# Kernel optimization log

Measured on AMD Instinct MI355X. Metric: run time of the kernel, lower is better.

## Reference

```python
import jax, jax.numpy as jnp
import numpy as np

T, E = 8192, 1024
LAYER_DEPTH, NUM_LAYERS = 12, 24


def _init_params():
    ratio_0_to_1 = LAYER_DEPTH / (NUM_LAYERS - 1)
    ratio_1_to_almost_0 = 1.0 - LAYER_DEPTH / NUM_LAYERS
    zigzag = 0.5 * (jnp.arange(1, E + 1) % 3 - 1)
    time_first = jnp.full(E, jnp.log(0.3), dtype=jnp.float32) + zigzag.astype(jnp.float32)
    h = jnp.arange(0, E, dtype=jnp.float32)
    time_decay = (-5 + 8 * (h / (E - 1)) ** (0.7 + 1.3 * ratio_0_to_1)).astype(jnp.float32)
    xr = jnp.arange(E, dtype=jnp.float32) / E
    time_mix_k = jnp.power(xr, ratio_1_to_almost_0)
    time_mix_v = time_mix_k + 0.3 * ratio_0_to_1
    time_mix_r = jnp.power(xr, 0.5 * ratio_1_to_almost_0)
    return time_first, time_decay, time_mix_k, time_mix_v, time_mix_r


def setup_inputs() -> dict:
    key = jax.random.key(0)
    kx, kk_, kv_, kr_, ko_ = jax.random.split(key, 5)
    scale = 1.0 / np.sqrt(E)
    tf, td, tmk, tmv, tmr = _init_params()
    return {
        "x": jax.random.normal(kx, (T, E), dtype=jnp.float32),
        "sx": jnp.zeros((E,), jnp.float32),
        "aa": jnp.zeros((E,), jnp.float32),
        "bb": jnp.zeros((E,), jnp.float32),
        "pp": jnp.zeros((E,), jnp.float32),
        "time_first": tf,
        "time_decay": td,
        "time_mix_k": tmk,
        "time_mix_v": tmv,
        "time_mix_r": tmr,
        "Wk": jax.random.normal(kk_, (E, E), jnp.float32) * scale,
        "Wv": jax.random.normal(kv_, (E, E), jnp.float32) * scale,
        "Wr": jax.random.normal(kr_, (E, E), jnp.float32) * scale,
        "Wo": jax.random.normal(ko_, (E, E), jnp.float32) * scale,
    }


def reference(x, sx, aa, bb, pp, time_first, time_decay,
              time_mix_k, time_mix_v, time_mix_r, Wk, Wv, Wr, Wo):
    # token-shift: previous token (or carried state sx at t=0)  [T, E]
    sx_seq = jnp.concatenate((sx[None, :], x[:-1, :]), axis=0)
    kx = x * time_mix_k + sx_seq * (1.0 - time_mix_k)
    vx = x * time_mix_v + sx_seq * (1.0 - time_mix_v)
    rx = x * time_mix_r + sx_seq * (1.0 - time_mix_r)

    r = jax.nn.sigmoid(rx @ Wr)  # [T, E]
    k = kx @ Wk                  # [T, E]
    v = vx @ Wv                  # [T, E]
    decay = -jnp.exp(time_decay)  # [E]

    def step(state, kv):
        aa_, bb_, pp_ = state
        kk, vv = kv
        ww = time_first + kk
        p = jnp.maximum(pp_, ww)
        e1 = jnp.exp(pp_ - p)
        e2 = jnp.exp(ww - p)
        out = (e1 * aa_ + e2 * vv) / (e1 * bb_ + e2)
        ww2 = decay + pp_
        p2 = jnp.maximum(ww2, kk)
        e1b = jnp.exp(ww2 - p2)
        e2b = jnp.exp(kk - p2)
        return (e1b * aa_ + e2b * vv, e1b * bb_ + e2b, p2), out

    (aa_f, bb_f, pp_f), wkv = jax.lax.scan(step, (aa, bb, pp), (k, v))
    out = x + (r * wkv) @ Wo
    return out, x[-1, :], aa_f, bb_f, pp_f
```

## Files before the change

### kernel.cpp

```cpp
#include <hip/hip_runtime.h>
#include <cstdint>
#include <cstddef>

typedef __bf16 bf16x8 __attribute__((ext_vector_type(8)));
typedef float  f32x4  __attribute__((ext_vector_type(4)));

#define TT 8192
#define EE 1024
#define NCHUNK 128
#define CLEN 64
#define LDSK 40

__device__ __forceinline__ unsigned short f2bf(float f) {
    union { float f; unsigned int u; } v; v.f = f;
    unsigned int r = v.u + 0x7FFFu + ((v.u >> 16) & 1u);
    return (unsigned short)(r >> 16);
}
__device__ __forceinline__ float b2f(unsigned int h) {
    union { unsigned int u; float f; } v; v.u = h << 16; return v.f;
}
__device__ __forceinline__ void gload_lds16(const void* g, void* l) {
    __builtin_amdgcn_global_load_lds((__attribute__((address_space(1))) void*)g,
                                     (__attribute__((address_space(3))) void*)l, 16, 0, 0);
}

__global__ void wt_kernel(const float* __restrict__ Wk, const float* __restrict__ Wv,
                          const float* __restrict__ Wr, const float* __restrict__ Wo,
                          unsigned short* __restrict__ Tk, unsigned short* __restrict__ Tv,
                          unsigned short* __restrict__ Tr, unsigned short* __restrict__ To) {
    __shared__ float tile[32][33];
    const float* W; unsigned short* D;
    switch (blockIdx.z) {
        case 0:  W = Wk; D = Tk; break;
        case 1:  W = Wv; D = Tv; break;
        case 2:  W = Wr; D = Tr; break;
        default: W = Wo; D = To; break;
    }
    const int bx = blockIdx.x * 32, by = blockIdx.y * 32;
    const int tx = threadIdx.x, ty = threadIdx.y;
#pragma unroll
    for (int r = 0; r < 4; ++r)
        tile[ty + 8 * r][tx] = W[(size_t)(by + ty + 8 * r) * EE + bx + tx];
    __syncthreads();
#pragma unroll
    for (int r = 0; r < 4; ++r)
        D[(size_t)(bx + ty + 8 * r) * EE + by + tx] = f2bf(tile[tx][ty + 8 * r]);
}

__global__ void prep_kernel(const float* __restrict__ Wk, const float* __restrict__ Wv,
                            const float* __restrict__ Wr, const float* __restrict__ Wo,
                            unsigned short* __restrict__ Tk, unsigned short* __restrict__ Tv,
                            unsigned short* __restrict__ Tr, unsigned short* __restrict__ To,
                            const float* __restrict__ x, const float* __restrict__ sx,
                            const float* __restrict__ tmk, const float* __restrict__ tmv,
                            const float* __restrict__ tmr,
                            unsigned short* __restrict__ kxb, unsigned short* __restrict__ vxb,
                            unsigned short* __restrict__ rxb) {
    const int bid = blockIdx.x;
    if (bid < 4096) {
        __shared__ float tile[32][33];
        const int z = bid >> 10;
        const float* W; unsigned short* D;
        switch (z) {
            case 0:  W = Wk; D = Tk; break;
            case 1:  W = Wv; D = Tv; break;
            case 2:  W = Wr; D = Tr; break;
            default: W = Wo; D = To; break;
        }
        const int by = ((bid >> 5) & 31) * 32, bx = (bid & 31) * 32;
        const int tx = threadIdx.x & 31, ty = threadIdx.x >> 5;
#pragma unroll
        for (int r = 0; r < 4; ++r)
            tile[ty + 8 * r][tx] = W[(size_t)(by + ty + 8 * r) * EE + bx + tx];
        __syncthreads();
#pragma unroll
        for (int r = 0; r < 4; ++r)
            D[(size_t)(bx + ty + 8 * r) * EE + by + tx] = f2bf(tile[tx][ty + 8 * r]);
    } else {
        const int gid  = (bid - 4096) * 256 + threadIdx.x;
        const int base = gid * 4;
        const int t = base >> 10;
        const int e = base & (EE - 1);
        float4 xv = *(const float4*)(x + base);
        float4 pv = (t > 0) ? *(const float4*)(x + base - EE) : *(const float4*)(sx + e);
        float4 mk = *(const float4*)(tmk + e);
        float4 mv = *(const float4*)(tmv + e);
        float4 mr = *(const float4*)(tmr + e);
        ushort4 ko, vo, ro;
        ko.x = f2bf(fmaf(mk.x, xv.x - pv.x, pv.x));
        ko.y = f2bf(fmaf(mk.y, xv.y - pv.y, pv.y));
        ko.z = f2bf(fmaf(mk.z, xv.z - pv.z, pv.z));
        ko.w = f2bf(fmaf(mk.w, xv.w - pv.w, pv.w));
        vo.x = f2bf(fmaf(mv.x, xv.x - pv.x, pv.x));
        vo.y = f2bf(fmaf(mv.y, xv.y - pv.y, pv.y));
        vo.z = f2bf(fmaf(mv.z, xv.z - pv.z, pv.z));
        vo.w = f2bf(fmaf(mv.w, xv.w - pv.w, pv.w));
        ro.x = f2bf(fmaf(mr.x, xv.x - pv.x, pv.x));
        ro.y = f2bf(fmaf(mr.y, xv.y - pv.y, pv.y));
        ro.z = f2bf(fmaf(mr.z, xv.z - pv.z, pv.z));
        ro.w = f2bf(fmaf(mr.w, xv.w - pv.w, pv.w));
        *(ushort4*)(kxb + base) = ko;
        *(ushort4*)(vxb + base) = vo;
        *(ushort4*)(rxb + base) = ro;
    }
}

__global__ __launch_bounds__(256, 2) void gemm_kvr3(
        const unsigned short* __restrict__ kxb, const unsigned short* __restrict__ vxb,
        const unsigned short* __restrict__ rxb,
        const unsigned short* __restrict__ Wkt, const unsigned short* __restrict__ Wvt,
        const unsigned short* __restrict__ Wrt,
        unsigned short* __restrict__ kf, unsigned short* __restrict__ vf,
        unsigned short* __restrict__ ry) {
    __shared__ __align__(16) unsigned short As[256 * 32];
    __shared__ __align__(16) unsigned short Bs[128 * 32];
    const int z = blockIdx.z;
    const unsigned short* A  = (z == 0) ? kxb : (z == 1) ? vxb : rxb;
    const unsigned short* Bt = (z == 0) ? Wkt : (z == 1) ? Wvt : Wrt;
    unsigned short* C        = (z == 0) ? kf  : (z == 1) ? vf  : ry;

    const int tid  = threadIdx.x;
    const int wave = tid >> 6, lane = tid & 63;
    const int wm = (wave >> 1) * 128, wn = (wave & 1) * 64;
    const int l15 = lane & 15, lq = lane >> 4;
    const int lrow = lane >> 2, lcol = (lane & 3) * 8;
    const int bm = blockIdx.x * 256, bn = blockIdx.y * 128;

    f32x4 acc[8][4] = {};

    for (int kt = 0; kt < 1024; kt += 32) {
        __syncthreads();
#pragma unroll
        for (int p = 0; p < 4; ++p) {
            const int r0 = p * 64 + wave * 16;
            gload_lds16(A + (size_t)(bm + r0 + lrow) * 1024 + kt + lcol, &As[r0 * 32]);
        }
#pragma unroll
        for (int p = 0; p < 2; ++p) {
            const int r0 = p * 64 + wave * 16;
            gload_lds16(Bt + (size_t)(bn + r0 + lrow) * 1024 + kt + lcol, &Bs[r0 * 32]);
        }
        __syncthreads();
        bf16x8 af[8], bfr[4];
#pragma unroll
        for (int i = 0; i < 8; ++i)
            af[i] = *(const bf16x8*)(&As[(wm + i * 16 + l15) * 32 + lq * 8]);
#pragma unroll
        for (int j = 0; j < 4; ++j)
            bfr[j] = *(const bf16x8*)(&Bs[(wn + j * 16 + l15) * 32 + lq * 8]);
#pragma unroll
        for (int i = 0; i < 8; ++i)
#pragma unroll
            for (int j = 0; j < 4; ++j)
                acc[i][j] = __builtin_amdgcn_mfma_f32_16x16x32_bf16(af[i], bfr[j], acc[i][j], 0, 0, 0);
    }

    const bool sig = (z == 2);
#pragma unroll
    for (int i = 0; i < 8; ++i)
#pragma unroll
        for (int j = 0; j < 4; ++j) {
            const int col = bn + wn + j * 16 + l15;
#pragma unroll
            for (int r = 0; r < 4; ++r) {
                const int row = bm + wm + i * 16 + lq * 4 + r;
                float val = acc[i][j][r];
                if (sig) val = 1.f / (1.f + __expf(-val));
                C[(size_t)row * 1024 + col] = f2bf(val);
            }
        }
}

__global__ __launch_bounds__(256, 2) void gemm_wo_big(const unsigned short* __restrict__ A,
                                                      const unsigned short* __restrict__ Bt,
                                                      const float* __restrict__ Res,
                                                      float* __restrict__ C) {
    __shared__ __align__(16) unsigned short As[256 * 32];
    __shared__ __align__(16) unsigned short Bs[128 * 32];
    const int tid  = threadIdx.x;
    const int wave = tid >> 6, lane = tid & 63;
    const int wm = (wave >> 1) * 128, wn = (wave & 1) * 64;
    const int l15 = lane & 15, lq = lane >> 4;
    const int lrow = lane >> 2, lcol = (lane & 3) * 8;
    const int bm = blockIdx.x * 256, bn = blockIdx.y * 128;

    f32x4 acc[8][4] = {};

    for (int kt = 0; kt < 1024; kt += 32) {
        __syncthreads();
#pragma unroll
        for (int p = 0; p < 4; ++p) {
            const int r0 = p * 64 + wave * 16;
            gload_lds16(A + (size_t)(bm + r0 + lrow) * 1024 + kt + lcol, &As[r0 * 32]);
        }
#pragma unroll
        for (int p = 0; p < 2; ++p) {
            const int r0 = p * 64 + wave * 16;
            gload_lds16(Bt + (size_t)(bn + r0 + lrow) * 1024 + kt + lcol, &Bs[r0 * 32]);
        }
        __syncthreads();
        bf16x8 af[8], bfr[4];
#pragma unroll
        for (int i = 0; i < 8; ++i)
            af[i] = *(const bf16x8*)(&As[(wm + i * 16 + l15) * 32 + lq * 8]);
#pragma unroll
        for (int j = 0; j < 4; ++j)
            bfr[j] = *(const bf16x8*)(&Bs[(wn + j * 16 + l15) * 32 + lq * 8]);
#pragma unroll
        for (int i = 0; i < 8; ++i)
#pragma unroll
            for (int j = 0; j < 4; ++j)
                acc[i][j] = __builtin_amdgcn_mfma_f32_16x16x32_bf16(af[i], bfr[j], acc[i][j], 0, 0, 0);
    }

#pragma unroll
    for (int i = 0; i < 8; ++i)
#pragma unroll
        for (int j = 0; j < 4; ++j) {
            const int col = bn + wn + j * 16 + l15;
#pragma unroll
            for (int r = 0; r < 4; ++r) {
                const int row = bm + wm + i * 16 + lq * 4 + r;
                const size_t idx = (size_t)row * 1024 + col;
                C[idx] = acc[i][j][r] + Res[idx];
            }
        }
}

__global__ __launch_bounds__(256) void gemm_bf(
        const unsigned short* __restrict__ A0, const unsigned short* __restrict__ B0,
        unsigned short* __restrict__ C0, const int sig0,
        const unsigned short* __restrict__ A1, const unsigned short* __restrict__ B1,
        unsigned short* __restrict__ C1, const int sig1) {
    __shared__ __align__(16) unsigned short As[128 * 32];
    __shared__ __align__(16) unsigned short Bs[128 * 32];
    const int z = blockIdx.z;
    const unsigned short* A  = z ? A1 : A0;
    const unsigned short* Bt = z ? B1 : B0;
    unsigned short* C        = z ? C1 : C0;
    const int sig            = z ? sig1 : sig0;

    const int tid  = threadIdx.x;
    const int wave = tid >> 6, lane = tid & 63;
    const int wm = (wave >> 1) * 64, wn = (wave & 1) * 64;
    const int l15 = lane & 15, lq = lane >> 4;
    const int lrow = lane >> 2, lcol = (lane & 3) * 8;
    const int bm = blockIdx.x * 128, bn = blockIdx.y * 128;

    f32x4 acc[4][4] = {};

    for (int kt = 0; kt < 1024; kt += 32) {
        __syncthreads();
#pragma unroll
        for (int p = 0; p < 2; ++p) {
            const int r0 = p * 64 + wave * 16;
            gload_lds16(A  + (size_t)(bm + r0 + lrow) * 1024 + kt + lcol, &As[r0 * 32]);
            gload_lds16(Bt + (size_t)(bn + r0 + lrow) * 1024 + kt + lcol, &Bs[r0 * 32]);
        }
        __syncthreads();
        bf16x8 af[4], bfr[4];
#pragma unroll
        for (int i = 0; i < 4; ++i) {
            af[i]  = *(const bf16x8*)(&As[(wm + i * 16 + l15) * 32 + lq * 8]);
            bfr[i] = *(const bf16x8*)(&Bs[(wn + i * 16 + l15) * 32 + lq * 8]);
        }
#pragma unroll
        for (int i = 0; i < 4; ++i)
#pragma unroll
            for (int j = 0; j < 4; ++j)
                acc[i][j] = __builtin_amdgcn_mfma_f32_16x16x32_bf16(af[i], bfr[j], acc[i][j], 0, 0, 0);
    }

#pragma unroll
    for (int i = 0; i < 4; ++i)
#pragma unroll
        for (int j = 0; j < 4; ++j) {
            const int col = bn + wn + j * 16 + l15;
#pragma unroll
            for (int r = 0; r < 4; ++r) {
                const int row = bm + wm + i * 16 + lq * 4 + r;
                float val = acc[i][j][r];
                if (sig) val = 1.f / (1.f + __expf(-val));
                C[(size_t)row * 1024 + col] = f2bf(val);
            }
        }
}

__global__ __launch_bounds__(256, 4) void gemm_kvr(
        const float* __restrict__ X, const float* __restrict__ SX,
        const float* __restrict__ tmk, const float* __restrict__ tmv,
        const float* __restrict__ tmr,
        const unsigned short* __restrict__ Wkt, const unsigned short* __restrict__ Wvt,
        const unsigned short* __restrict__ Wrt,
        unsigned short* __restrict__ outK, unsigned short* __restrict__ outV,
        unsigned short* __restrict__ outR) {
    __shared__ __align__(16) unsigned short As[128 * LDSK];
    __shared__ __align__(16) unsigned short Bs[128 * LDSK];
    const int z = blockIdx.z;
    const float* TM = (z == 0) ? tmk : (z == 1) ? tmv : tmr;
    const unsigned short* Bt = (z == 0) ? Wkt : (z == 1) ? Wvt : Wrt;
    unsigned short* Cout = (z == 0) ? outK : (z == 1) ? outV : outR;

    const int tid  = threadIdx.x;
    const int wave = tid >> 6, lane = tid & 63;
    const int wm = (wave >> 1) * 64, wn = (wave & 1) * 64;
    const int l15 = lane & 15, lq = lane >> 4;
    const int bm = blockIdx.x * 128, bn = blockIdx.y * 128;

    f32x4 acc[4][4] = {};

    for (int kt = 0; kt < 1024; kt += 32) {
        __syncthreads();
#pragma unroll
        for (int p = 0; p < 2; ++p) {
            const int li  = p * 256 + tid;
            const int row = li >> 2, q = li & 3;
            const int e0  = kt + q * 8;
            {
                const int t = bm + row;
                const float* xr = X + (size_t)t * EE + e0;
                const float* pr = (t > 0) ? (X + (size_t)(t - 1) * EE + e0) : (SX + e0);
                float4 xa = *(const float4*)xr, xb = *(const float4*)(xr + 4);
                float4 pa = *(const float4*)pr, pb = *(const float4*)(pr + 4);
                float4 ma = *(const float4*)(TM + e0), mb = *(const float4*)(TM + e0 + 4);
                ushort4 lo, hi;
                lo.x = f2bf(fmaf(ma.x, xa.x - pa.x, pa.x));
                lo.y = f2bf(fmaf(ma.y, xa.y - pa.y, pa.y));
                lo.z = f2bf(fmaf(ma.z, xa.z - pa.z, pa.z));
                lo.w = f2bf(fmaf(ma.w, xa.w - pa.w, pa.w));
                hi.x = f2bf(fmaf(mb.x, xb.x - pb.x, pb.x));
                hi.y = f2bf(fmaf(mb.y, xb.y - pb.y, pb.y));
                hi.z = f2bf(fmaf(mb.z, xb.z - pb.z, pb.z));
                hi.w = f2bf(fmaf(mb.w, xb.w - pb.w, pb.w));
                *(ushort4*)(&As[row * LDSK + q * 8])     = lo;
                *(ushort4*)(&As[row * LDSK + q * 8 + 4]) = hi;
            }
            *(uint4*)(&Bs[row * LDSK + q * 8]) =
                *(const uint4*)(Bt + (size_t)(bn + row) * 1024 + e0);
        }
        __syncthreads();
        bf16x8 af[4], bfr[4];
#pragma unroll
        for (int i = 0; i < 4; ++i) {
            af[i]  = *(const bf16x8*)(&As[(wm + i * 16 + l15) * LDSK + lq * 8]);
            bfr[i] = *(const bf16x8*)(&Bs[(wn + i * 16 + l15) * LDSK + lq * 8]);
        }
#pragma unroll
        for (int i = 0; i < 4; ++i)
#pragma unroll
            for (int j = 0; j < 4; ++j)
                acc[i][j] = __builtin_amdgcn_mfma_f32_16x16x32_bf16(af[i], bfr[j], acc[i][j], 0, 0, 0);
    }

    const bool sig = (z == 2);
#pragma unroll
    for (int i = 0; i < 4; ++i)
#pragma unroll
        for (int j = 0; j < 4; ++j) {
            const int col = bn + wn + j * 16 + l15;
#pragma unroll
            for (int r = 0; r < 4; ++r) {
                const int row = bm + wm + i * 16 + lq * 4 + r;
                float val = acc[i][j][r];
                if (sig) val = 1.f / (1.f + __expf(-val));
                Cout[(size_t)row * 1024 + col] = f2bf(val);
            }
        }
}

__global__ void wkv_pass_a(const unsigned short* __restrict__ k,
                           const unsigned short* __restrict__ v,
                           const float* __restrict__ td,
                           float* __restrict__ Sa, float* __restrict__ Sb, float* __restrict__ Sp) {
    const int gid = blockIdx.x * 256 + threadIdx.x;
    const int c = gid >> 10, e = gid & (EE - 1);
    const float w = -__expf(td[e]);
    float sa = 0.f, sb = 0.f, sp = -1e30f;
    const size_t base = (size_t)c * CLEN * EE + e;
    for (int i = 0; i < CLEN; ++i) {
        const size_t idx = base + (size_t)i * EE;
        const float kk = b2f(k[idx]), vv = b2f(v[idx]);
        const float q  = fmaf(w, (float)(CLEN - 1 - i), kk);
        const float p2 = fmaxf(sp, q);
        const float e1 = __expf(sp - p2), e2 = __expf(q - p2);
        sa = fmaf(e1, sa, e2 * vv);
        sb = fmaf(e1, sb, e2);
        sp = p2;
    }
    Sa[gid] = sa; Sb[gid] = sb; Sp[gid] = sp;
}

__global__ void wkv_pass_b(const float* __restrict__ aa, const float* __restrict__ bb,
                           const float* __restrict__ pp, const float* __restrict__ td,
                           const float* __restrict__ x,
                           const float* __restrict__ Sa, const float* __restrict__ Sb,
                           const float* __restrict__ Sp,
                           float* __restrict__ ina, float* __restrict__ inb,
                           float* __restrict__ inp, float* __restrict__ outTail) {
    const int e = blockIdx.x * 256 + threadIdx.x;
    const float w  = -__expf(td[e]);
    const float wL = w * (float)CLEN;
    float a = aa[e], b = bb[e], p = pp[e];
    for (int c = 0; c < NCHUNK; ++c) {
        const int idx = c * EE + e;
        ina[idx] = a; inb[idx] = b; inp[idx] = p;
        const float sa = Sa[idx], sb = Sb[idx], sp = Sp[idx];
        const float pw = p + wL;
        const float p2 = fmaxf(pw, sp);
        const float e1 = __expf(pw - p2), e2 = __expf(sp - p2);
        a = fmaf(e1, a, e2 * sa);
        b = fmaf(e1, b, e2 * sb);
        p = p2;
    }
    outTail[e]          = x[(size_t)(TT - 1) * EE + e];
    outTail[EE + e]     = a;
    outTail[2 * EE + e] = b;
    outTail[3 * EE + e] = p;
}

__global__ void wkv_pass_c(const unsigned short* __restrict__ k,
                           const unsigned short* __restrict__ v,
                           const float* __restrict__ tf, const float* __restrict__ td,
                           const float* __restrict__ ina, const float* __restrict__ inb,
                           const float* __restrict__ inp,
                           unsigned short* ry) {
    const int gid = blockIdx.x * 256 + threadIdx.x;
    const int c = gid >> 10, e = gid & (EE - 1);
    const float w = -__expf(td[e]);
    const float u = tf[e];
    float a = ina[gid], b = inb[gid], p = inp[gid];
    const size_t base = (size_t)c * CLEN * EE + e;
    for (int i = 0; i < CLEN; ++i) {
        const size_t idx = base + (size_t)i * EE;
        const float kk = b2f(k[idx]), vv = b2f(v[idx]);
        const float rr = b2f(ry[idx]);
        const float ww = u + kk;
        const float pq = fmaxf(p, ww);
        const float e1 = __expf(p - pq), e2 = __expf(ww - pq);
        const float wkv = fmaf(e1, a, e2 * vv) / fmaf(e1, b, e2);
        ry[idx] = f2bf(rr * wkv);
        const float ww2 = w + p;
        const float p2  = fmaxf(ww2, kk);
        const float e1b = __expf(ww2 - p2), e2b = __expf(kk - p2);
        a = fmaf(e1b, a, e2b * vv);
        b = fmaf(e1b, b, e2b);
        p = p2;
    }
}

extern "C" void kernel_launch(void* const* d_in, const int* in_sizes, int n_in,
                              void* d_out, int out_size, void* d_ws, size_t ws_size,
                              hipStream_t stream) {
    const float* x   = (const float*)d_in[0];
    const float* sx  = (const float*)d_in[1];
    const float* aa  = (const float*)d_in[2];
    const float* bb  = (const float*)d_in[3];
    const float* pp  = (const float*)d_in[4];
    const float* tf  = (const float*)d_in[5];
    const float* td  = (const float*)d_in[6];
    const float* tmk = (const float*)d_in[7];
    const float* tmv = (const float*)d_in[8];
    const float* tmr = (const float*)d_in[9];
    const float* Wk  = (const float*)d_in[10];
    const float* Wv  = (const float*)d_in[11];
    const float* Wr  = (const float*)d_in[12];
    const float* Wo  = (const float*)d_in[13];
    float* out = (float*)d_out;

    char* ws = (char*)d_ws;
    const size_t MB = 1ull << 20;
    const size_t QK = (size_t)NCHUNK * EE * sizeof(float);

    unsigned short* Wkt = (unsigned short*)(ws + 0 * MB);
    unsigned short* Wvt = (unsigned short*)(ws + 2 * MB);
    unsigned short* Wrt = (unsigned short*)(ws + 4 * MB);
    unsigned short* Wot = (unsigned short*)(ws + 6 * MB);

    if (ws_size >= 75 * MB) {
        unsigned short* rxb = (unsigned short*)(ws + 8 * MB);
        unsigned short* kf  = (unsigned short*)(ws + 24 * MB);
        unsigned short* ry  = (unsigned short*)(ws + 40 * MB);
        unsigned short* vf  = (unsigned short*)(ws + 56 * MB);
        char* scan = ws + 72 * MB;
        float* Sa  = (float*)(scan);
        float* Sb  = (float*)(scan + QK);
        float* Sp  = (float*)(scan + 2 * QK);
        float* ina = (float*)(scan + 3 * QK);
        float* inb = (float*)(scan + 4 * QK);
        float* inp = (float*)(scan + 5 * QK);
        unsigned short* kxb = (unsigned short*)d_out;
        unsigned short* vxb = (unsigned short*)d_out + (size_t)TT * EE;

        prep_kernel<<<12288, 256, 0, stream>>>(Wk, Wv, Wr, Wo, Wkt, Wvt, Wrt, Wot,
                                               x, sx, tmk, tmv, tmr, kxb, vxb, rxb);
        gemm_kvr3<<<dim3(32, 8, 3), 256, 0, stream>>>(kxb, vxb, rxb, Wkt, Wvt, Wrt, kf, vf, ry);
        wkv_pass_a<<<(NCHUNK * EE) / 256, 256, 0, stream>>>(kf, vf, td, Sa, Sb, Sp);
        wkv_pass_b<<<4, 256, 0, stream>>>(aa, bb, pp, td, x, Sa, Sb, Sp, ina, inb, inp,
                                          out + (size_t)TT * EE);
        wkv_pass_c<<<(NCHUNK * EE) / 256, 256, 0, stream>>>(kf, vf, tf, td, ina, inb, inp, ry);
        gemm_wo_big<<<dim3(32, 8), 256, 0, stream>>>(ry, Wot, x, out);
    } else if (ws_size >= 59 * MB) {
        unsigned short* rxb = (unsigned short*)(ws + 8 * MB);
        unsigned short* kf  = (unsigned short*)(ws + 24 * MB);
        unsigned short* ry  = (unsigned short*)(ws + 40 * MB);
        char* scan = ws + 56 * MB;
        float* Sa  = (float*)(scan);
        float* Sb  = (float*)(scan + QK);
        float* Sp  = (float*)(scan + 2 * QK);
        float* ina = (float*)(scan + 3 * QK);
        float* inb = (float*)(scan + 4 * QK);
        float* inp = (float*)(scan + 5 * QK);
        unsigned short* kxb = (unsigned short*)d_out;
        unsigned short* vxb = (unsigned short*)d_out + (size_t)TT * EE;
        unsigned short* vf  = kxb;

        prep_kernel<<<12288, 256, 0, stream>>>(Wk, Wv, Wr, Wo, Wkt, Wvt, Wrt, Wot,
                                               x, sx, tmk, tmv, tmr, kxb, vxb, rxb);
        gemm_bf<<<dim3(64, 8, 2), 256, 0, stream>>>(kxb, Wkt, kf, 0, rxb, Wrt, ry, 1);
        gemm_bf<<<dim3(64, 8, 1), 256, 0, stream>>>(vxb, Wvt, vf, 0, nullptr, nullptr, nullptr, 0);
        wkv_pass_a<<<(NCHUNK * EE) / 256, 256, 0, stream>>>(kf, vf, td, Sa, Sb, Sp);
        wkv_pass_b<<<4, 256, 0, stream>>>(aa, bb, pp, td, x, Sa, Sb, Sp, ina, inb, inp,
                                          out + (size_t)TT * EE);
        wkv_pass_c<<<(NCHUNK * EE) / 256, 256, 0, stream>>>(kf, vf, tf, td, ina, inb, inp, ry);
        gemm_wo_big<<<dim3(32, 8), 256, 0, stream>>>(ry, Wot, x, out);
    } else {
        unsigned short* ry = (unsigned short*)(ws + 8 * MB);
        char* scan = ws + 24 * MB;
        float* Sa  = (float*)(scan);
        float* Sb  = (float*)(scan + QK);
        float* Sp  = (float*)(scan + 2 * QK);
        float* ina = (float*)(scan + 3 * QK);
        float* inb = (float*)(scan + 4 * QK);
        float* inp = (float*)(scan + 5 * QK);
        unsigned short* kf = (unsigned short*)d_out;
        unsigned short* vf = (unsigned short*)d_out + (size_t)TT * EE;

        wt_kernel<<<dim3(32, 32, 4), dim3(32, 8), 0, stream>>>(Wk, Wv, Wr, Wo, Wkt, Wvt, Wrt, Wot);
        gemm_kvr<<<dim3(64, 8, 3), 256, 0, stream>>>(x, sx, tmk, tmv, tmr,
                                                     Wkt, Wvt, Wrt, kf, vf, ry);
        wkv_pass_a<<<(NCHUNK * EE) / 256, 256, 0, stream>>>(kf, vf, td, Sa, Sb, Sp);
        wkv_pass_b<<<4, 256, 0, stream>>>(aa, bb, pp, td, x, Sa, Sb, Sp, ina, inb, inp,
                                          out + (size_t)TT * EE);
        wkv_pass_c<<<(NCHUNK * EE) / 256, 256, 0, stream>>>(kf, vf, tf, td, ina, inb, inp, ry);
        gemm_wo_big<<<dim3(32, 8), 256, 0, stream>>>(ry, Wot, x, out);
    }
}
```

Baseline: 287.3 us.

## Double-buffer GEMM LDS tiles and parallelize chunked WKV scan

```diff
diff --git a/kernel.cpp b/kernel.cpp
--- a/kernel.cpp
+++ b/kernel.cpp
@@ -7,8 +7,6 @@
 
 #define TT 8192
 #define EE 1024
-#define NCHUNK 128
-#define CLEN 64
 #define LDSK 40
 
 __device__ __forceinline__ unsigned short f2bf(float f) {
@@ -105,15 +103,15 @@
     }
 }
 
-__global__ __launch_bounds__(256, 2) void gemm_kvr3(
+__global__ __launch_bounds__(256, 2) void gemm_kvr3_db(
         const unsigned short* __restrict__ kxb, const unsigned short* __restrict__ vxb,
         const unsigned short* __restrict__ rxb,
         const unsigned short* __restrict__ Wkt, const unsigned short* __restrict__ Wvt,
         const unsigned short* __restrict__ Wrt,
         unsigned short* __restrict__ kf, unsigned short* __restrict__ vf,
         unsigned short* __restrict__ ry) {
-    __shared__ __align__(16) unsigned short As[256 * 32];
-    __shared__ __align__(16) unsigned short Bs[128 * 32];
+    __shared__ __align__(16) unsigned short As[2][256 * 32];
+    __shared__ __align__(16) unsigned short Bs[2][128 * 32];
     const int z = blockIdx.z;
     const unsigned short* A  = (z == 0) ? kxb : (z == 1) ? vxb : rxb;
     const unsigned short* Bt = (z == 0) ? Wkt : (z == 1) ? Wvt : Wrt;
@@ -128,32 +126,36 @@
 
     f32x4 acc[8][4] = {};
 
-    for (int kt = 0; kt < 1024; kt += 32) {
-        __syncthreads();
-#pragma unroll
-        for (int p = 0; p < 4; ++p) {
-            const int r0 = p * 64 + wave * 16;
-            gload_lds16(A + (size_t)(bm + r0 + lrow) * 1024 + kt + lcol, &As[r0 * 32]);
-        }
-#pragma unroll
-        for (int p = 0; p < 2; ++p) {
-            const int r0 = p * 64 + wave * 16;
-            gload_lds16(Bt + (size_t)(bn + r0 + lrow) * 1024 + kt + lcol, &Bs[r0 * 32]);
-        }
-        __syncthreads();
+#define STAGE_KVR(kt, dst) {                                                      \
+    _Pragma("unroll") for (int p = 0; p < 4; ++p) {                               \
+        const int r0 = p * 64 + wave * 16;                                        \
+        gload_lds16(A + (size_t)(bm + r0 + lrow) * 1024 + (kt) + lcol,            \
+                    &As[dst][r0 * 32]); }                                         \
+    _Pragma("unroll") for (int p = 0; p < 2; ++p) {                               \
+        const int r0 = p * 64 + wave * 16;                                        \
+        gload_lds16(Bt + (size_t)(bn + r0 + lrow) * 1024 + (kt) + lcol,           \
+                    &Bs[dst][r0 * 32]); } }
+
+    STAGE_KVR(0, 0);
+    for (int it = 0; it < 32; ++it) {
+        asm volatile("s_waitcnt vmcnt(0)" ::: "memory");
+        __syncthreads();
+        const int cur = it & 1;
+        if (it < 31) STAGE_KVR((it + 1) * 32, cur ^ 1);
         bf16x8 af[8], bfr[4];
 #pragma unroll
         for (int i = 0; i < 8; ++i)
-            af[i] = *(const bf16x8*)(&As[(wm + i * 16 + l15) * 32 + lq * 8]);
+            af[i] = *(const bf16x8*)(&As[cur][(wm + i * 16 + l15) * 32 + lq * 8]);
 #pragma unroll
         for (int j = 0; j < 4; ++j)
-            bfr[j] = *(const bf16x8*)(&Bs[(wn + j * 16 + l15) * 32 + lq * 8]);
+            bfr[j] = *(const bf16x8*)(&Bs[cur][(wn + j * 16 + l15) * 32 + lq * 8]);
 #pragma unroll
         for (int i = 0; i < 8; ++i)
 #pragma unroll
             for (int j = 0; j < 4; ++j)
                 acc[i][j] = __builtin_amdgcn_mfma_f32_16x16x32_bf16(af[i], bfr[j], acc[i][j], 0, 0, 0);
     }
+#undef STAGE_KVR
 
     const bool sig = (z == 2);
 #pragma unroll
@@ -171,12 +173,12 @@
         }
 }
 
-__global__ __launch_bounds__(256, 2) void gemm_wo_big(const unsigned short* __restrict__ A,
-                                                      const unsigned short* __restrict__ Bt,
-                                                      const float* __restrict__ Res,
-                                                      float* __restrict__ C) {
-    __shared__ __align__(16) unsigned short As[256 * 32];
-    __shared__ __align__(16) unsigned short Bs[128 * 32];
+__global__ __launch_bounds__(256, 2) void gemm_wo_db(const unsigned short* __restrict__ A,
+                                                     const unsigned short* __restrict__ Bt,
+                                                     const float* __restrict__ Res,
+                                                     float* __restrict__ C) {
+    __shared__ __align__(16) unsigned short As[2][256 * 32];
+    __shared__ __align__(16) unsigned short Bs[2][128 * 32];
     const int tid  = threadIdx.x;
     const int wave = tid >> 6, lane = tid & 63;
     const int wm = (wave >> 1) * 128, wn = (wave & 1) * 64;
@@ -186,32 +188,36 @@
 
     f32x4 acc[8][4] = {};
 
-    for (int kt = 0; kt < 1024; kt += 32) {
-        __syncthreads();
-#pragma unroll
-        for (int p = 0; p < 4; ++p) {
-            const int r0 = p * 64 + wave * 16;
-            gload_lds16(A + (size_t)(bm + r0 + lrow) * 1024 + kt + lcol, &As[r0 * 32]);
-        }
-#pragma unroll
-        for (int p = 0; p < 2; ++p) {
-            const int r0 = p * 64 + wave * 16;
-            gload_lds16(Bt + (size_t)(bn + r0 + lrow) * 1024 + kt + lcol, &Bs[r0 * 32]);
-        }
-        __syncthreads();
+#define STAGE_WO(kt, dst) {                                                       \
+    _Pragma("unroll") for (int p = 0; p < 4; ++p) {                               \
+        const int r0 = p * 64 + wave * 16;                                        \
+        gload_lds16(A + (size_t)(bm + r0 + lrow) * 1024 + (kt) + lcol,            \
+                    &As[dst][r0 * 32]); }                                         \
+    _Pragma("unroll") for (int p = 0; p < 2; ++p) {                               \
+        const int r0 = p * 64 + wave * 16;                                        \
+        gload_lds16(Bt + (size_t)(bn + r0 + lrow) * 1024 + (kt) + lcol,           \
+                    &Bs[dst][r0 * 32]); } }
+
+    STAGE_WO(0, 0);
+    for (int it = 0; it < 32; ++it) {
+        asm volatile("s_waitcnt vmcnt(0)" ::: "memory");
+        __syncthreads();
+        const int cur = it & 1;
+        if (it < 31) STAGE_WO((it + 1) * 32, cur ^ 1);
         bf16x8 af[8], bfr[4];
 #pragma unroll
         for (int i = 0; i < 8; ++i)
-            af[i] = *(const bf16x8*)(&As[(wm + i * 16 + l15) * 32 + lq * 8]);
+            af[i] = *(const bf16x8*)(&As[cur][(wm + i * 16 + l15) * 32 + lq * 8]);
 #pragma unroll
         for (int j = 0; j < 4; ++j)
-            bfr[j] = *(const bf16x8*)(&Bs[(wn + j * 16 + l15) * 32 + lq * 8]);
+            bfr[j] = *(const bf16x8*)(&Bs[cur][(wn + j * 16 + l15) * 32 + lq * 8]);
 #pragma unroll
         for (int i = 0; i < 8; ++i)
 #pragma unroll
             for (int j = 0; j < 4; ++j)
                 acc[i][j] = __builtin_amdgcn_mfma_f32_16x16x32_bf16(af[i], bfr[j], acc[i][j], 0, 0, 0);
     }
+#undef STAGE_WO
 
 #pragma unroll
     for (int i = 0; i < 8; ++i)
@@ -227,63 +233,147 @@
         }
 }
 
-__global__ __launch_bounds__(256) void gemm_bf(
-        const unsigned short* __restrict__ A0, const unsigned short* __restrict__ B0,
-        unsigned short* __restrict__ C0, const int sig0,
-        const unsigned short* __restrict__ A1, const unsigned short* __restrict__ B1,
-        unsigned short* __restrict__ C1, const int sig1) {
-    __shared__ __align__(16) unsigned short As[128 * 32];
-    __shared__ __align__(16) unsigned short Bs[128 * 32];
-    const int z = blockIdx.z;
-    const unsigned short* A  = z ? A1 : A0;
-    const unsigned short* Bt = z ? B1 : B0;
-    unsigned short* C        = z ? C1 : C0;
-    const int sig            = z ? sig1 : sig0;
-
-    const int tid  = threadIdx.x;
-    const int wave = tid >> 6, lane = tid & 63;
-    const int wm = (wave >> 1) * 64, wn = (wave & 1) * 64;
-    const int l15 = lane & 15, lq = lane >> 4;
-    const int lrow = lane >> 2, lcol = (lane & 3) * 8;
-    const int bm = blockIdx.x * 128, bn = blockIdx.y * 128;
-
-    f32x4 acc[4][4] = {};
-
-    for (int kt = 0; kt < 1024; kt += 32) {
-        __syncthreads();
-#pragma unroll
-        for (int p = 0; p < 2; ++p) {
-            const int r0 = p * 64 + wave * 16;
-            gload_lds16(A  + (size_t)(bm + r0 + lrow) * 1024 + kt + lcol, &As[r0 * 32]);
-            gload_lds16(Bt + (size_t)(bn + r0 + lrow) * 1024 + kt + lcol, &Bs[r0 * 32]);
-        }
-        __syncthreads();
-        bf16x8 af[4], bfr[4];
-#pragma unroll
-        for (int i = 0; i < 4; ++i) {
-            af[i]  = *(const bf16x8*)(&As[(wm + i * 16 + l15) * 32 + lq * 8]);
-            bfr[i] = *(const bf16x8*)(&Bs[(wn + i * 16 + l15) * 32 + lq * 8]);
-        }
-#pragma unroll
-        for (int i = 0; i < 4; ++i)
-#pragma unroll
-            for (int j = 0; j < 4; ++j)
-                acc[i][j] = __builtin_amdgcn_mfma_f32_16x16x32_bf16(af[i], bfr[j], acc[i][j], 0, 0, 0);
-    }
-
-#pragma unroll
-    for (int i = 0; i < 4; ++i)
-#pragma unroll
-        for (int j = 0; j < 4; ++j) {
-            const int col = bn + wn + j * 16 + l15;
-#pragma unroll
-            for (int r = 0; r < 4; ++r) {
-                const int row = bm + wm + i * 16 + lq * 4 + r;
-                float val = acc[i][j][r];
-                if (sig) val = 1.f / (1.f + __expf(-val));
-                C[(size_t)row * 1024 + col] = f2bf(val);
-            }
-        }
+template <int NC>
+__global__ void wkv_pass_a(const unsigned short* __restrict__ k,
+                           const unsigned short* __restrict__ v,
+                           const float* __restrict__ td,
+                           float* __restrict__ Sa, float* __restrict__ Sb, float* __restrict__ Sp) {
+    const int CL = TT / NC;
+    const int gid = blockIdx.x * 256 + threadIdx.x;
+    const int c = gid >> 10, e = gid & (EE - 1);
+    const float w = -__expf(td[e]);
+    float sa = 0.f, sb = 0.f, sp = -1e30f;
+    const size_t base = (size_t)c * CL * EE + e;
+    for (int i = 0; i < CL; ++i) {
+        const size_t idx = base + (size_t)i * EE;
+        const float kk = b2f(k[idx]), vv = b2f(v[idx]);
+        const float q  = fmaf(w, (float)(CL - 1 - i), kk);
+        const float p2 = fmaxf(sp, q);
+        const float e1 = __expf(sp - p2), e2 = __expf(q - p2);
+        sa = fmaf(e1, sa, e2 * vv);
+        sb = fmaf(e1, sb, e2);
+        sp = p2;
+    }
+    Sa[gid] = sa; Sb[gid] = sb; Sp[gid] = sp;
+}
+
+__global__ void wkv_pass_b_par(const float* __restrict__ aa, const float* __restrict__ bb,
+                               const float* __restrict__ pp, const float* __restrict__ td,
+                               const float* __restrict__ x,
+                               const float* __restrict__ Sa, const float* __restrict__ Sb,
+                               const float* __restrict__ Sp,
+                               float* __restrict__ ina, float* __restrict__ inb,
+                               float* __restrict__ inp, float* __restrict__ outTail) {
+    const int NC = 256, CL = TT / NC;
+    const int e = blockIdx.x, c = threadIdx.x;
+    __shared__ float sA[256], sB[256], sP[256];
+    const float w = -__expf(td[e]);
+
+    float a = Sa[c * EE + e], b = Sb[c * EE + e], p = Sp[c * EE + e];
+
+    for (int s = 1; s < NC; s <<= 1) {
+        sA[c] = a; sB[c] = b; sP[c] = p;
+        __syncthreads();
+        if (c >= s) {
+            const float myLen = (float)(CL * min(c + 1, s));
+            const float aL = sA[c - s], bL = sB[c - s], pL = sP[c - s];
+            const float pLd = pL + w * myLen;
+            const float pn  = fmaxf(pLd, p);
+            const float e1  = __expf(pLd - pn), e2 = __expf(p - pn);
+            a = fmaf(e1, aL, e2 * a);
+            b = fmaf(e1, bL, e2 * b);
+            p = pn;
+        }
+        __syncthreads();
+    }
+
+    sA[c] = a; sB[c] = b; sP[c] = p;
+    __syncthreads();
+
+    const float a0 = aa[e], b0 = bb[e], p0 = pp[e];
+    float ea, eb, ep;
+    if (c == 0) { ea = a0; eb = b0; ep = p0; }
+    else {
+        const float aL = sA[c - 1], bL = sB[c - 1], pL = sP[c - 1];
+        const float p0d = p0 + w * (float)(c * CL);
+        const float pn  = fmaxf(p0d, pL);
+        const float e1  = __expf(p0d - pn), e2 = __expf(pL - pn);
+        ea = fmaf(e1, a0, e2 * aL);
+        eb = fmaf(e1, b0, e2 * bL);
+        ep = pn;
+    }
+    ina[e * NC + c] = ea; inb[e * NC + c] = eb; inp[e * NC + c] = ep;
+
+    if (c == NC - 1) {
+        const float p0d = p0 + w * (float)TT;
+        const float pn  = fmaxf(p0d, p);
+        const float e1  = __expf(p0d - pn), e2 = __expf(p - pn);
+        outTail[e]          = x[(size_t)(TT - 1) * EE + e];
+        outTail[EE + e]     = fmaf(e1, a0, e2 * a);
+        outTail[2 * EE + e] = fmaf(e1, b0, e2 * b);
+        outTail[3 * EE + e] = pn;
+    }
+}
+
+template <int NC>
+__global__ void wkv_pass_c(const unsigned short* __restrict__ k,
+                           const unsigned short* __restrict__ v,
+                           const float* __restrict__ tf, const float* __restrict__ td,
+                           const float* __restrict__ ina, const float* __restrict__ inb,
+                           const float* __restrict__ inp,
+                           unsigned short* ry) {
+    const int CL = TT / NC;
+    const int gid = blockIdx.x * 256 + threadIdx.x;
+    const int c = gid >> 10, e = gid & (EE - 1);
+    const float w = -__expf(td[e]);
+    const float u = tf[e];
+    float a = ina[e * NC + c], b = inb[e * NC + c], p = inp[e * NC + c];
+    const size_t base = (size_t)c * CL * EE + e;
+    for (int i = 0; i < CL; ++i) {
+        const size_t idx = base + (size_t)i * EE;
+        const float kk = b2f(k[idx]), vv = b2f(v[idx]);
+        const float rr = b2f(ry[idx]);
+        const float ww = u + kk;
+        const float pq = fmaxf(p, ww);
+        const float e1 = __expf(p - pq), e2 = __expf(ww - pq);
+        const float wkv = fmaf(e1, a, e2 * vv) / fmaf(e1, b, e2);
+        ry[idx] = f2bf(rr * wkv);
+        const float ww2 = w + p;
+        const float p2  = fmaxf(ww2, kk);
+        const float e1b = __expf(ww2 - p2), e2b = __expf(kk - p2);
+        a = fmaf(e1b, a, e2b * vv);
+        b = fmaf(e1b, b, e2b);
+        p = p2;
+    }
+}
+
+__global__ void wkv_pass_b_small(const float* __restrict__ aa, const float* __restrict__ bb,
+                                 const float* __restrict__ pp, const float* __restrict__ td,
+                                 const float* __restrict__ x,
+                                 const float* __restrict__ Sa, const float* __restrict__ Sb,
+                                 const float* __restrict__ Sp,
+                                 float* __restrict__ ina, float* __restrict__ inb,
+                                 float* __restrict__ inp, float* __restrict__ outTail) {
+    const int NC = 128, CL = TT / NC;
+    const int e = blockIdx.x * 256 + threadIdx.x;
+    const float w  = -__expf(td[e]);
+    const float wL = w * (float)CL;
+    float a = aa[e], b = bb[e], p = pp[e];
+    for (int c = 0; c < NC; ++c) {
+        ina[e * NC + c] = a; inb[e * NC + c] = b; inp[e * NC + c] = p;
+        const int idx = c * EE + e;
+        const float sa = Sa[idx], sb = Sb[idx], sp = Sp[idx];
+        const float pw = p + wL;
+        const float p2 = fmaxf(pw, sp);
+        const float e1 = __expf(pw - p2), e2 = __expf(sp - p2);
+        a = fmaf(e1, a, e2 * sa);
+        b = fmaf(e1, b, e2 * sb);
+        p = p2;
+    }
+    outTail[e]          = x[(size_t)(TT - 1) * EE + e];
+    outTail[EE + e]     = a;
+    outTail[2 * EE + e] = b;
+    outTail[3 * EE + e] = p;
 }
 
 __global__ __launch_bounds__(256, 4) void gemm_kvr(
@@ -368,86 +458,6 @@
         }
 }
 
-__global__ void wkv_pass_a(const unsigned short* __restrict__ k,
-                           const unsigned short* __restrict__ v,
-                           const float* __restrict__ td,
-                           float* __restrict__ Sa, float* __restrict__ Sb, float* __restrict__ Sp) {
-    const int gid = blockIdx.x * 256 + threadIdx.x;
-    const int c = gid >> 10, e = gid & (EE - 1);
-    const float w = -__expf(td[e]);
-    float sa = 0.f, sb = 0.f, sp = -1e30f;
-    const size_t base = (size_t)c * CLEN * EE + e;
-    for (int i = 0; i < CLEN; ++i) {
-        const size_t idx = base + (size_t)i * EE;
-        const float kk = b2f(k[idx]), vv = b2f(v[idx]);
-        const float q  = fmaf(w, (float)(CLEN - 1 - i), kk);
-        const float p2 = fmaxf(sp, q);
-        const float e1 = __expf(sp - p2), e2 = __expf(q - p2);
-        sa = fmaf(e1, sa, e2 * vv);
-        sb = fmaf(e1, sb, e2);
-        sp = p2;
-    }
-    Sa[gid] = sa; Sb[gid] = sb; Sp[gid] = sp;
-}
-
-__global__ void wkv_pass_b(const float* __restrict__ aa, const float* __restrict__ bb,
-                           const float* __restrict__ pp, const float* __restrict__ td,
-                           const float* __restrict__ x,
-                           const float* __restrict__ Sa, const float* __restrict__ Sb,
-                           const float* __restrict__ Sp,
-                           float* __restrict__ ina, float* __restrict__ inb,
-                           float* __restrict__ inp, float* __restrict__ outTail) {
-    const int e = blockIdx.x * 256 + threadIdx.x;
-    const float w  = -__expf(td[e]);
-    const float wL = w * (float)CLEN;
-    float a = aa[e], b = bb[e], p = pp[e];
-    for (int c = 0; c < NCHUNK; ++c) {
-        const int idx = c * EE + e;
-        ina[idx] = a; inb[idx] = b; inp[idx] = p;
-        const float sa = Sa[idx], sb = Sb[idx], sp = Sp[idx];
-        const float pw = p + wL;
-        const float p2 = fmaxf(pw, sp);
-        const float e1 = __expf(pw - p2), e2 = __expf(sp - p2);
-        a = fmaf(e1, a, e2 * sa);
-        b = fmaf(e1, b, e2 * sb);
-        p = p2;
-    }
-    outTail[e]          = x[(size_t)(TT - 1) * EE + e];
-    outTail[EE + e]     = a;
-    outTail[2 * EE + e] = b;
-    outTail[3 * EE + e] = p;
-}
-
-__global__ void wkv_pass_c(const unsigned short* __restrict__ k,
-                           const unsigned short* __restrict__ v,
-                           const float* __restrict__ tf, const float* __restrict__ td,
-                           const float* __restrict__ ina, const float* __restrict__ inb,
-                           const float* __restrict__ inp,
-                           unsigned short* ry) {
-    const int gid = blockIdx.x * 256 + threadIdx.x;
-    const int c = gid >> 10, e = gid & (EE - 1);
-    const float w = -__expf(td[e]);
-    const float u = tf[e];
-    float a = ina[gid], b = inb[gid], p = inp[gid];
-    const size_t base = (size_t)c * CLEN * EE + e;
-    for (int i = 0; i < CLEN; ++i) {
-        const size_t idx = base + (size_t)i * EE;
-        const float kk = b2f(k[idx]), vv = b2f(v[idx]);
-        const float rr = b2f(ry[idx]);
-        const float ww = u + kk;
-        const float pq = fmaxf(p, ww);
-        const float e1 = __expf(p - pq), e2 = __expf(ww - pq);
-        const float wkv = fmaf(e1, a, e2 * vv) / fmaf(e1, b, e2);
-        ry[idx] = f2bf(rr * wkv);
-        const float ww2 = w + p;
-        const float p2  = fmaxf(ww2, kk);
-        const float e1b = __expf(ww2 - p2), e2b = __expf(kk - p2);
-        a = fmaf(e1b, a, e2b * vv);
-        b = fmaf(e1b, b, e2b);
-        p = p2;
-    }
-}
-
 extern "C" void kernel_launch(void* const* d_in, const int* in_sizes, int n_in,
                               void* d_out, int out_size, void* d_ws, size_t ws_size,
                               hipStream_t stream) {
@@ -469,7 +479,6 @@
 
     char* ws = (char*)d_ws;
     const size_t MB = 1ull << 20;
-    const size_t QK = (size_t)NCHUNK * EE * sizeof(float);
 
     unsigned short* Wkt = (unsigned short*)(ws + 0 * MB);
     unsigned short* Wvt = (unsigned short*)(ws + 2 * MB);
@@ -481,51 +490,29 @@
         unsigned short* kf  = (unsigned short*)(ws + 24 * MB);
         unsigned short* ry  = (unsigned short*)(ws + 40 * MB);
         unsigned short* vf  = (unsigned short*)(ws + 56 * MB);
-        char* scan = ws + 72 * MB;
-        float* Sa  = (float*)(scan);
-        float* Sb  = (float*)(scan + QK);
-        float* Sp  = (float*)(scan + 2 * QK);
-        float* ina = (float*)(scan + 3 * QK);
-        float* inb = (float*)(scan + 4 * QK);
-        float* inp = (float*)(scan + 5 * QK);
+        float* Sa  = (float*)(ws + 8 * MB);
+        float* Sb  = (float*)(ws + 9 * MB);
+        float* Sp  = (float*)(ws + 10 * MB);
+        float* ina = (float*)(ws + 11 * MB);
+        float* inb = (float*)(ws + 12 * MB);
+        float* inp = (float*)(ws + 13 * MB);
         unsigned short* kxb = (unsigned short*)d_out;
         unsigned short* vxb = (unsigned short*)d_out + (size_t)TT * EE;
 
         prep_kernel<<<12288, 256, 0, stream>>>(Wk, Wv, Wr, Wo, Wkt, Wvt, Wrt, Wot,
                                                x, sx, tmk, tmv, tmr, kxb, vxb, rxb);
-        gemm_kvr3<<<dim3(32, 8, 3), 256, 0, stream>>>(kxb, vxb, rxb, Wkt, Wvt, Wrt, kf, vf, ry);
-        wkv_pass_a<<<(NCHUNK * EE) / 256, 256, 0, stream>>>(kf, vf, td, Sa, Sb, Sp);
-        wkv_pass_b<<<4, 256, 0, stream>>>(aa, bb, pp, td, x, Sa, Sb, Sp, ina, inb, inp,
-                                          out + (size_t)TT * EE);
-        wkv_pass_c<<<(NCHUNK * EE) / 256, 256, 0, stream>>>(kf, vf, tf, td, ina, inb, inp, ry);
-        gemm_wo_big<<<dim3(32, 8), 256, 0, stream>>>(ry, Wot, x, out);
-    } else if (ws_size >= 59 * MB) {
-        unsigned short* rxb = (unsigned short*)(ws + 8 * MB);
-        unsigned short* kf  = (unsigned short*)(ws + 24 * MB);
-        unsigned short* ry  = (unsigned short*)(ws + 40 * MB);
-        char* scan = ws + 56 * MB;
-        float* Sa  = (float*)(scan);
-        float* Sb  = (float*)(scan + QK);
-        float* Sp  = (float*)(scan + 2 * QK);
-        float* ina = (float*)(scan + 3 * QK);
-        float* inb = (float*)(scan + 4 * QK);
-        float* inp = (float*)(scan + 5 * QK);
-        unsigned short* kxb = (unsigned short*)d_out;
-        unsigned short* vxb = (unsigned short*)d_out + (size_t)TT * EE;
-        unsigned short* vf  = kxb;
-
-        prep_kernel<<<12288, 256, 0, stream>>>(Wk, Wv, Wr, Wo, Wkt, Wvt, Wrt, Wot,
-                                               x, sx, tmk, tmv, tmr, kxb, vxb, rxb);
-        gemm_bf<<<dim3(64, 8, 2), 256, 0, stream>>>(kxb, Wkt, kf, 0, rxb, Wrt, ry, 1);
-        gemm_bf<<<dim3(64, 8, 1), 256, 0, stream>>>(vxb, Wvt, vf, 0, nullptr, nullptr, nullptr, 0);
-        wkv_pass_a<<<(NCHUNK * EE) / 256, 256, 0, stream>>>(kf, vf, td, Sa, Sb, Sp);
-        wkv_pass_b<<<4, 256, 0, stream>>>(aa, bb, pp, td, x, Sa, Sb, Sp, ina, inb, inp,
-                                          out + (size_t)TT * EE);
-        wkv_pass_c<<<(NCHUNK * EE) / 256, 256, 0, stream>>>(kf, vf, tf, td, ina, inb, inp, ry);
-        gemm_wo_big<<<dim3(32, 8), 256, 0, stream>>>(ry, Wot, x, out);
+        gemm_kvr3_db<<<dim3(32, 8, 3), 256, 0, stream>>>(kxb, vxb, rxb, Wkt, Wvt, Wrt,
+                                                         kf, vf, ry);
+        wkv_pass_a<256><<<(256 * EE) / 256, 256, 0, stream>>>(kf, vf, td, Sa, Sb, Sp);
+        wkv_pass_b_par<<<EE, 256, 0, stream>>>(aa, bb, pp, td, x, Sa, Sb, Sp,
+                                               ina, inb, inp, out + (size_t)TT * EE);
+        wkv_pass_c<256><<<(256 * EE) / 256, 256, 0, stream>>>(kf, vf, tf, td,
+                                                              ina, inb, inp, ry);
+        gemm_wo_db<<<dim3(32, 8), 256, 0, stream>>>(ry, Wot, x, out);
     } else {
         unsigned short* ry = (unsigned short*)(ws + 8 * MB);
         char* scan = ws + 24 * MB;
+        const size_t QK = (size_t)128 * EE * sizeof(float);
         float* Sa  = (float*)(scan);
         float* Sb  = (float*)(scan + QK);
         float* Sp  = (float*)(scan + 2 * QK);
@@ -538,10 +525,11 @@
         wt_kernel<<<dim3(32, 32, 4), dim3(32, 8), 0, stream>>>(Wk, Wv, Wr, Wo, Wkt, Wvt, Wrt, Wot);
         gemm_kvr<<<dim3(64, 8, 3), 256, 0, stream>>>(x, sx, tmk, tmv, tmr,
                                                      Wkt, Wvt, Wrt, kf, vf, ry);
-        wkv_pass_a<<<(NCHUNK * EE) / 256, 256, 0, stream>>>(kf, vf, td, Sa, Sb, Sp);
-        wkv_pass_b<<<4, 256, 0, stream>>>(aa, bb, pp, td, x, Sa, Sb, Sp, ina, inb, inp,
-                                          out + (size_t)TT * EE);
-        wkv_pass_c<<<(NCHUNK * EE) / 256, 256, 0, stream>>>(kf, vf, tf, td, ina, inb, inp, ry);
-        gemm_wo_big<<<dim3(32, 8), 256, 0, stream>>>(ry, Wot, x, out);
-    }
-}
+        wkv_pass_a<128><<<(128 * EE) / 256, 256, 0, stream>>>(kf, vf, td, Sa, Sb, Sp);
+        wkv_pass_b_small<<<4, 256, 0, stream>>>(aa, bb, pp, td, x, Sa, Sb, Sp,
+                                                ina, inb, inp, out + (size_t)TT * EE);
+        wkv_pass_c<128><<<(128 * EE) / 256, 256, 0, stream>>>(kf, vf, tf, td,
+                                                              ina, inb, inp, ry);
+        gemm_wo_db<<<dim3(32, 8), 256, 0, stream>>>(ry, Wot, x, out);
+    }
+}
```

After: 294.0 us. 2.3% more time.
